# Performance work log

Measured on AMD Instinct MI355X. Metric: run time of the kernel, lower is better.

The kernel has to match this reference:

```python
import jax, jax.numpy as jnp
import numpy as np

NUM_HEADS = 16

def setup_inputs() -> dict:
    key = jax.random.key(0)
    ks = jax.random.split(key, 9)
    B, N, D = 4, 4096, 1024
    s = 1.0 / np.sqrt(D)
    return {
        "x": jax.random.normal(ks[0], (B, N, D), dtype=jnp.float32),
        "Wq": jax.random.normal(ks[1], (D, D), dtype=jnp.float32) * s,
        "bq": jnp.zeros((D,), dtype=jnp.float32),
        "Wk": jax.random.normal(ks[2], (D, D), dtype=jnp.float32) * s,
        "bk": jnp.zeros((D,), dtype=jnp.float32),
        "Wv": jax.random.normal(ks[3], (D, D), dtype=jnp.float32) * s,
        "bv": jnp.zeros((D,), dtype=jnp.float32),
        "Wp": jax.random.normal(ks[4], (D, D), dtype=jnp.float32) * s,
        "bp": jnp.zeros((D,), dtype=jnp.float32),
    }

def _split_heads(t, H):
    B, N, D = t.shape
    return t.reshape(B, N, H, D // H).transpose(0, 2, 1, 3)  # [B,H,N,hd]

def reference(x, Wq, bq, Wk, bk, Wv, bv, Wp, bp):
    H = NUM_HEADS
    q = jax.nn.elu(x @ Wq + bq) + 1.0   # elu feature map (config.elu=True)
    k = jax.nn.elu(x @ Wk + bk) + 1.0
    v = x @ Wv + bv
    q, k, v = _split_heads(q, H), _split_heads(k, H), _split_heads(v, H)
    # k^T v: [B,H,hd,hd]
    kv = jnp.einsum('bhnd,bhne->bhde', k, v)
    numerator = jnp.einsum('bhnd,bhde->bhne', q, kv)  # [B,H,N,hd]
    # adaptive normalizer: q @ sum_k
    sum_k = k.sum(axis=2)  # [B,H,hd]
    denominator = jnp.einsum('bhnd,bhd->bhn', q, sum_k)[..., None]
    y = numerator / denominator
    B, _, N, hd = y.shape
    y = y.transpose(0, 2, 1, 3).reshape(B, N, H * hd)
    return y @ Wp + bp
```

## Files before the change

kernel.cpp:

```cpp
#include <hip/hip_runtime.h>
#include <hip/hip_bf16.h>

typedef __attribute__((ext_vector_type(4))) float f32x4;
typedef __attribute__((ext_vector_type(4))) short s16x4;
typedef __attribute__((ext_vector_type(8))) short s16x8;
typedef __attribute__((ext_vector_type(8))) __bf16 bf16x8;

#define DEV static __device__ __forceinline__

DEV float bf2f(ushort u){
  unsigned x = ((unsigned)u) << 16;
  return __builtin_bit_cast(float, x);
}
DEV ushort f2bf(float f){
  unsigned x = __builtin_bit_cast(unsigned, f);
  x += 0x7fffu + ((x >> 16) & 1u);
  return (ushort)(x >> 16);
}
DEV void load_lds16(const void* g, void* l){
  __builtin_amdgcn_global_load_lds((const __attribute__((address_space(1))) void*)g,
                                   (__attribute__((address_space(3))) void*)l, 16, 0, 0);
}

__global__ __launch_bounds__(256) void k_prep(
    const float* __restrict__ x, ushort* __restrict__ xb,
    const float* __restrict__ Wq, const float* __restrict__ Wk,
    const float* __restrict__ Wv, const float* __restrict__ Wp,
    ushort* __restrict__ qkvT, ushort* __restrict__ wpT)
{
  __shared__ float tile[32][33];
  int bid = blockIdx.x, tid = threadIdx.x;
  if (bid < 8192) {
    int i = bid * 256 + tid;
    const f32x4* p = (const f32x4*)(x + (size_t)i * 8);
    f32x4 a = p[0], b = p[1];
    s16x8 o;
    o[0]=(short)f2bf(a[0]); o[1]=(short)f2bf(a[1]); o[2]=(short)f2bf(a[2]); o[3]=(short)f2bf(a[3]);
    o[4]=(short)f2bf(b[0]); o[5]=(short)f2bf(b[1]); o[6]=(short)f2bf(b[2]); o[7]=(short)f2bf(b[3]);
    *(s16x8*)(xb + (size_t)i * 8) = o;
  } else {
    int r = bid - 8192;
    int z = r >> 10; r &= 1023;
    const float* W = (z == 0) ? Wq : (z == 1) ? Wk : (z == 2) ? Wv : Wp;
    ushort* out = (z < 3) ? (qkvT + (size_t)z * 1024 * 1024) : wpT;
    int bx = (r & 31) * 32, by = (r >> 5) * 32;
    int tx = tid & 31, ty = tid >> 5;
    #pragma unroll
    for (int j = 0; j < 32; j += 8)
      tile[ty + j][tx] = W[(size_t)(by + ty + j) * 1024 + bx + tx];
    __syncthreads();
    #pragma unroll
    for (int j = 0; j < 32; j += 8)
      out[(size_t)(bx + ty + j) * 1024 + by + tx] = f2bf(tile[tx][ty + j]);
  }
}

template<int MODE>
__global__ __launch_bounds__(512, 1) void k_gemm(
    const ushort* __restrict__ A, const ushort* __restrict__ Bt,
    const float* __restrict__ b0, const float* __restrict__ b1, const float* __restrict__ b2,
    ushort* __restrict__ oQ, ushort* __restrict__ oK, ushort* __restrict__ oV,
    float* __restrict__ oF, int N)
{
  const int K = 1024;
  __shared__ ushort ldsA[2][16384];
  __shared__ ushort ldsB[2][16384];

  int wg = blockIdx.x;
  int cpx = gridDim.x >> 3;
  wg = (wg & 7) * cpx + (wg >> 3);
  int nbn = N >> 8;
  int bmi = wg / nbn, bni = wg - bmi * nbn;
  int m0 = bmi << 8, n0 = bni << 8;
  int tid = threadIdx.x, wid = tid >> 6, lane = tid & 63;
  int wr = wid >> 2, wc = wid & 3;
  int hi = lane >> 4, L = lane & 15;

  int rr = tid >> 3;
  int gaA = ((tid & 7) ^ (rr & 7)) << 3;
  int gaB = ((tid & 7) ^ ((tid >> 5) & 7)) << 3;
  const ushort* gA = A  + (size_t)(m0 + rr) * K + gaA;
  const ushort* gB = Bt + (size_t)(n0 + rr) * K + gaB;
  int ldst = wid << 10;

  int swz = (hi ^ (L & 7)) << 4;
  int arow = (wr * 128 + L) << 7;
  int brow = ((wc * 64 + L * 4)) << 7;

  f32x4 acc[8][4] = {};
  bf16x8 af[4], bf[4];

  #define RD_A(BASE, MH, KX)                                                   \
    _Pragma("unroll")                                                          \
    for (int m = 0; m < 4; ++m)                                                \
      af[m] = *(const bf16x8*)((BASE) + arow + (MH) * 8192 + (m << 11) + (swz ^ (KX)));
  #define RD_B(BASE, KX)                                                       \
    _Pragma("unroll")                                                          \
    for (int n = 0; n < 4; ++n)                                                \
      bf[n] = *(const bf16x8*)((BASE) + brow + (n << 7) + (swz ^ (KX)));
  #define MFMA16(MOFF)                                                         \
    _Pragma("unroll")                                                          \
    for (int m = 0; m < 4; ++m)                                                \
      _Pragma("unroll")                                                        \
      for (int n = 0; n < 4; ++n)                                              \
        acc[m + (MOFF)][n] =                                                   \
          __builtin_amdgcn_mfma_f32_16x16x32_bf16(af[m], bf[n], acc[m + (MOFF)][n], 0, 0, 0);

  #define ST_A0(SA_, kof) load_lds16(gA + (kof),                   (SA_) + ldst);
  #define ST_A1(SA_, kof) load_lds16(gA + (size_t) 64 * K + (kof), (SA_) + 8192  + ldst);
  #define ST_A2(SA_, kof) load_lds16(gA + (size_t)128 * K + (kof), (SA_) + 16384 + ldst);
  #define ST_A3(SA_, kof) load_lds16(gA + (size_t)192 * K + (kof), (SA_) + 24576 + ldst);
  #define ST_B0(SB_, kof) load_lds16(gB + (kof),                   (SB_) + ldst);
  #define ST_B1(SB_, kof) load_lds16(gB + (size_t) 64 * K + (kof), (SB_) + 8192  + ldst);
  #define ST_B2(SB_, kof) load_lds16(gB + (size_t)128 * K + (kof), (SB_) + 16384 + ldst);
  #define ST_B3(SB_, kof) load_lds16(gB + (size_t)192 * K + (kof), (SB_) + 24576 + ldst);

  #define PH8(LA_, LB_, MH, KX, MOFF, STG, WAIT)                               \
  { STG                                                                        \
    WAIT                                                                       \
    RD_A(LA_, MH, KX)                                                          \
    RD_B(LB_, KX)                                                              \
    asm volatile("s_waitcnt lgkmcnt(0)" ::: "memory");                         \
    __builtin_amdgcn_sched_barrier(0);                                         \
    __builtin_amdgcn_s_setprio(1);                                             \
    MFMA16(MOFF)                                                               \
    __builtin_amdgcn_s_setprio(0);                                             \
    __builtin_amdgcn_s_barrier(); }

  #define W2 { asm volatile("s_waitcnt vmcnt(2)" ::: "memory"); __builtin_amdgcn_s_barrier(); }
  #define W0 { asm volatile("s_waitcnt vmcnt(0)" ::: "memory"); __builtin_amdgcn_s_barrier(); }

  char* SA0 = (char*)&ldsA[0][0];
  char* SA1 = (char*)&ldsA[1][0];
  char* SB0 = (char*)&ldsB[0][0];
  char* SB1 = (char*)&ldsB[1][0];
  const char* LA0 = (const char*)&ldsA[0][0];
  const char* LA1 = (const char*)&ldsA[1][0];
  const char* LB0 = (const char*)&ldsB[0][0];
  const char* LB1 = (const char*)&ldsB[1][0];

  ST_A0(SA0, 0) ST_A1(SA0, 0) ST_A2(SA0, 0) ST_A3(SA0, 0)
  ST_B0(SB0, 0) ST_B1(SB0, 0) ST_B2(SB0, 0) ST_B3(SB0, 0)

  for (int i = 0; i < 7; ++i) {
    size_t ko  = (size_t)(2 * i + 1) << 6;
    size_t ke2 = (size_t)(2 * i + 2) << 6;
    PH8(LA0, LB0, 0, 0,  0, { ST_A1(SA1, ko) ST_A3(SA1, ko) }, W2)
    PH8(LA0, LB0, 0, 64, 0, { ST_A0(SA1, ko) ST_A2(SA1, ko) }, )
    PH8(LA0, LB0, 1, 64, 4, { ST_B0(SB1, ko) ST_B1(SB1, ko) }, )
    PH8(LA0, LB0, 1, 0,  4, { ST_B2(SB1, ko) ST_B3(SB1, ko) }, )
    PH8(LA1, LB1, 0, 0,  0, { ST_A1(SA0, ke2) ST_A3(SA0, ke2) }, W2)
    PH8(LA1, LB1, 0, 64, 0, { ST_A0(SA0, ke2) ST_A2(SA0, ke2) }, )
    PH8(LA1, LB1, 1, 64, 4, { ST_B0(SB0, ke2) ST_B1(SB0, ke2) }, )
    PH8(LA1, LB1, 1, 0,  4, { ST_B2(SB0, ke2) ST_B3(SB0, ke2) }, )
  }
  {
    size_t ko = (size_t)15 << 6;
    PH8(LA0, LB0, 0, 0,  0, { ST_A1(SA1, ko) ST_A3(SA1, ko) }, W2)
    PH8(LA0, LB0, 0, 64, 0, { ST_A0(SA1, ko) ST_A2(SA1, ko) }, )
    PH8(LA0, LB0, 1, 64, 4, { ST_B0(SB1, ko) ST_B1(SB1, ko) }, )
    PH8(LA0, LB0, 1, 0,  4, { ST_B2(SB1, ko) ST_B3(SB1, ko) }, )
    PH8(LA1, LB1, 0, 0,  0, { }, W0)
    PH8(LA1, LB1, 0, 64, 0, { }, )
    PH8(LA1, LB1, 1, 64, 4, { }, )
    PH8(LA1, LB1, 1, 0,  4, { }, )
  }
  #undef PH8
  #undef W2
  #undef W0
  #undef RD_A
  #undef RD_B
  #undef MFMA16

  int row0 = m0 + wr * 128 + (hi << 2);
  int cb4 = n0 + wc * 64 + (L << 2);
  if constexpr (MODE == 0) {
    f32x4 bias; ushort* dst; bool act;
    if (cb4 < 1024)      { bias = *(const f32x4*)(b0 + cb4);          dst = oQ + cb4;          act = true;  }
    else if (cb4 < 2048) { bias = *(const f32x4*)(b1 + (cb4 - 1024)); dst = oK + (cb4 - 1024); act = true;  }
    else                 { bias = *(const f32x4*)(b2 + (cb4 - 2048)); dst = oV + (cb4 - 2048); act = false; }
    #pragma unroll
    for (int m = 0; m < 8; ++m)
      #pragma unroll
      for (int j = 0; j < 4; ++j) {
        int r = row0 + m * 16 + j;
        s16x4 w;
        #pragma unroll
        for (int n = 0; n < 4; ++n) {
          float v = acc[m][n][j] + bias[n];
          if (act) v = (v > 0.f) ? (v + 1.f) : __expf(v);
          w[n] = (short)f2bf(v);
        }
        *(s16x4*)(dst + (size_t)r * 1024) = w;
      }
  } else {
    f32x4 bias = *(const f32x4*)(b0 + cb4);
    #pragma unroll
    for (int m = 0; m < 8; ++m)
      #pragma unroll
      for (int j = 0; j < 4; ++j) {
        int r = row0 + m * 16 + j;
        f32x4 w;
        #pragma unroll
        for (int n = 0; n < 4; ++n) w[n] = acc[m][n][j] + bias[n];
        *(f32x4*)(oF + (size_t)r * 1024 + cb4) = w;
      }
  }
}

__global__ __launch_bounds__(256, 2) void k_kv(
    const ushort* __restrict__ kbuf, const ushort* __restrict__ vbuf,
    float* __restrict__ kvp, float* __restrict__ skp)
{
  __shared__ ushort tile[2][8192];
  __shared__ float red[64 * 68];
  __shared__ float skred[4][64];

  int bh = blockIdx.x >> 3, chunk = blockIdx.x & 7;
  int b = bh >> 4, h = bh & 15;
  int tid = threadIdx.x, wid = tid >> 6, lane = tid & 63;
  int d0 = (lane >> 3) << 3, e0 = (lane & 7) << 3;

  size_t gbase = ((size_t)b * 4096 + chunk * 512 + wid * 16 + (lane >> 3)) * 1024
               + h * 64 + (lane & 7) * 8;

  float acc[8][8] = {};
  float sk[8] = {};

  #define STAGE_KV(bp, c)                                                     \
  { char* base_ = (char*)&tile[bp][0] + (wid << 11);                          \
    size_t g_ = gbase + (size_t)(c) * 65536;                                  \
    load_lds16(kbuf + g_,        base_);                                      \
    load_lds16(kbuf + g_ + 8192, base_ + 1024);                               \
    load_lds16(vbuf + g_,        base_ + 8192);                               \
    load_lds16(vbuf + g_ + 8192, base_ + 9216); }

  STAGE_KV(0, 0)

  for (int c = 0; c < 8; ++c) {
    if (c + 1 < 8) {
      STAGE_KV((c + 1) & 1, c + 1)
      asm volatile("s_waitcnt vmcnt(4)" ::: "memory");
    } else {
      asm volatile("s_waitcnt vmcnt(0)" ::: "memory");
    }
    __builtin_amdgcn_s_barrier();
    const ushort* Ks = &tile[c & 1][0];
    const ushort* Vs = &tile[c & 1][4096];
    #pragma unroll
    for (int t = 0; t < 16; ++t) {
      int nn = (wid << 4) + t;
      s16x8 k8 = *(const s16x8*)(Ks + nn * 64 + d0);
      s16x8 v8 = *(const s16x8*)(Vs + nn * 64 + e0);
      float kf[8], vf[8];
      #pragma unroll
      for (int i = 0; i < 8; ++i) { kf[i] = bf2f((ushort)k8[i]); vf[i] = bf2f((ushort)v8[i]); }
      #pragma unroll
      for (int i = 0; i < 8; ++i) {
        sk[i] += kf[i];
        #pragma unroll
        for (int j = 0; j < 8; ++j) acc[i][j] += kf[i] * vf[j];
      }
    }
    __builtin_amdgcn_sched_barrier(0);
    __builtin_amdgcn_s_barrier();
  }
  #undef STAGE_KV

  for (int w = 0; w < 4; ++w) {
    if (wid == w) {
      #pragma unroll
      for (int i = 0; i < 8; ++i)
        #pragma unroll
        for (int j4 = 0; j4 < 2; ++j4) {
          f32x4 v4;
          v4[0] = acc[i][j4 * 4 + 0]; v4[1] = acc[i][j4 * 4 + 1];
          v4[2] = acc[i][j4 * 4 + 2]; v4[3] = acc[i][j4 * 4 + 3];
          float* p = &red[(d0 + i) * 68 + e0 + j4 * 4];
          if (w == 0) *(f32x4*)p = v4;
          else        { f32x4 o = *(const f32x4*)p; *(f32x4*)p = o + v4; }
        }
    }
    __syncthreads();
  }

  size_t kvbase = ((size_t)chunk * 64 + bh) * 4096;
  #pragma unroll
  for (int i = 0; i < 16; ++i) {
    int el = tid + i * 256;
    kvp[kvbase + el] = red[(el >> 6) * 68 + (el & 63)];
  }
  if ((lane & 7) == 0) {
    #pragma unroll
    for (int i = 0; i < 8; ++i) skred[wid][d0 + i] = sk[i];
  }
  __syncthreads();
  if (tid < 64) {
    float s = 0.f;
    #pragma unroll
    for (int w = 0; w < 4; ++w) s += skred[w][tid];
    skp[(((size_t)chunk * 64 + bh) << 6) + tid] = s;
  }
}

__global__ __launch_bounds__(512, 2) void k_num(
    const ushort* __restrict__ qbuf, const float* __restrict__ kvp,
    const float* __restrict__ skp, ushort* __restrict__ ybuf)
{
  __shared__ float kvf[4096];
  __shared__ ushort kvtb[4096];
  __shared__ ushort skb[64];

  int bh = blockIdx.x >> 3, chunk = blockIdx.x & 7;
  int b = bh >> 4, h = bh & 15;
  int tid = threadIdx.x, wid = tid >> 6, lane = tid & 63;
  int hi = lane >> 4, L = lane & 15;

  #pragma unroll
  for (int i = 0; i < 2; ++i) {
    int i4 = tid + i * 512;
    f32x4 s = {0.f, 0.f, 0.f, 0.f};
    #pragma unroll
    for (int sl = 0; sl < 8; ++sl)
      s += *(const f32x4*)&kvp[(((size_t)sl * 64 + bh) << 12) + ((size_t)i4 << 2)];
    *(f32x4*)&kvf[i4 << 2] = s;
  }
  if (tid < 64) {
    float s = 0.f;
    #pragma unroll
    for (int sl = 0; sl < 8; ++sl) s += skp[(((size_t)sl * 64 + bh) << 6) + tid];
    skb[tid] = f2bf(s);
  }
  __syncthreads();
  {
    int e = tid >> 3, dg = tid & 7;
    s16x8 o;
    #pragma unroll
    for (int j = 0; j < 8; ++j) o[j] = (short)f2bf(kvf[(dg * 8 + j) * 64 + e]);
    *(s16x8*)((char*)kvtb + e * 128 + ((dg ^ (e & 7)) << 4)) = o;
  }
  __syncthreads();

  size_t r0 = (size_t)b * 4096 + chunk * 512 + wid * 64;
  const ushort* qb = qbuf + (r0 + L) * 1024 + h * 64 + hi * 8;

  f32x4 acc[4][4] = {};
  f32x4 accd[4] = {};
  #pragma unroll
  for (int kk = 0; kk < 2; ++kk) {
    bf16x8 bfr[4], bfd;
    bfd = *(const bf16x8*)((const char*)skb + kk * 64 + hi * 16);
    #pragma unroll
    for (int n = 0; n < 4; ++n) {
      int e = L * 4 + n;
      bfr[n] = *(const bf16x8*)((char*)kvtb + e * 128 + ((((kk << 2) | hi) ^ (e & 7)) << 4));
    }
    #pragma unroll
    for (int m = 0; m < 4; ++m) {
      bf16x8 af = *(const bf16x8*)(qb + (size_t)m * 16 * 1024 + kk * 32);
      #pragma unroll
      for (int n = 0; n < 4; ++n)
        acc[m][n] = __builtin_amdgcn_mfma_f32_16x16x32_bf16(af, bfr[n], acc[m][n], 0, 0, 0);
      accd[m] = __builtin_amdgcn_mfma_f32_16x16x32_bf16(af, bfd, accd[m], 0, 0, 0);
    }
  }

  #pragma unroll
  for (int m = 0; m < 4; ++m)
    #pragma unroll
    for (int j = 0; j < 4; ++j) {
      float inv = 1.0f / accd[m][j];
      s16x4 w;
      #pragma unroll
      for (int n = 0; n < 4; ++n) w[n] = (short)f2bf(acc[m][n][j] * inv);
      *(s16x4*)(ybuf + (r0 + m * 16 + hi * 4 + j) * 1024 + h * 64 + L * 4) = w;
    }
}

extern "C" void kernel_launch(void* const* d_in, const int* in_sizes, int n_in,
                              void* d_out, int out_size, void* d_ws, size_t ws_size,
                              hipStream_t stream)
{
  const float* x  = (const float*)d_in[0];
  const float* Wq = (const float*)d_in[1];
  const float* bq = (const float*)d_in[2];
  const float* Wk = (const float*)d_in[3];
  const float* bk = (const float*)d_in[4];
  const float* Wv = (const float*)d_in[5];
  const float* bv = (const float*)d_in[6];
  const float* Wp = (const float*)d_in[7];
  const float* bp = (const float*)d_in[8];

  char* ws = (char*)d_ws;
  ushort* xb    = (ushort*)(ws + 0);
  ushort* qkvT  = (ushort*)(ws + 33554432);
  ushort* wpT   = (ushort*)(ws + 39845888);
  ushort* ybuf  = (ushort*)(ws + 41943040);
  float*  kvp   = (float*)(ws + 0);
  float*  skp   = (float*)(ws + 8388608);

  ushort* vbuf = (ushort*)d_out;
  ushort* qbuf = (ushort*)d_out + 16777216;
  ushort* kbuf = ybuf;

  k_prep<<<12288, 256, 0, stream>>>(x, xb, Wq, Wk, Wv, Wp, qkvT, wpT);
  k_gemm<0><<<768, 512, 0, stream>>>(xb, qkvT, bq, bk, bv, qbuf, kbuf, vbuf, nullptr, 3072);
  k_kv<<<512, 256, 0, stream>>>(kbuf, vbuf, kvp, skp);
  k_num<<<512, 512, 0, stream>>>(qbuf, kvp, skp, ybuf);
  k_gemm<1><<<256, 512, 0, stream>>>(ybuf, wpT, bp, nullptr, nullptr,
                                     nullptr, nullptr, nullptr, (float*)d_out, 1024);
}
```

Before: 265.6 us.

## Restructure GEMM main loop into quadrant phases with deeper A prefetch

Reorganizes the 256x256 bf16 GEMM k-loop so each phase reads both k-halves of an A or B fragment set and issues MFMAs per output quadrant (8 phases per 2 k-tiles), reusing loaded fragments across phases. The global-to-LDS staging is rescheduled: A for the next tile is prefetched two tiles ahead, B loads are grouped, and vmcnt waits are moved to the end of phases. The aim is fewer LDS reads per MFMA and better overlap of global loads with compute, at the cost of more fragment registers and a more intricate barrier/wait ordering that could race if the counts are wrong.

```diff
diff --git a/kernel.cpp b/kernel.cpp
--- a/kernel.cpp
+++ b/kernel.cpp
@@ -88,47 +88,52 @@
   int brow = ((wc * 64 + L * 4)) << 7;
 
   f32x4 acc[8][4] = {};
-  bf16x8 af[4], bf[4];
-
-  #define RD_A(BASE, MH, KX)                                                   \
-    _Pragma("unroll")                                                          \
-    for (int m = 0; m < 4; ++m)                                                \
-      af[m] = *(const bf16x8*)((BASE) + arow + (MH) * 8192 + (m << 11) + (swz ^ (KX)));
-  #define RD_B(BASE, KX)                                                       \
-    _Pragma("unroll")                                                          \
-    for (int n = 0; n < 4; ++n)                                                \
-      bf[n] = *(const bf16x8*)((BASE) + brow + (n << 7) + (swz ^ (KX)));
-  #define MFMA16(MOFF)                                                         \
+  bf16x8 af[4][2];
+  bf16x8 bf[4][2];
+
+  #define RD_A(BASE, MH)                                                       \
     _Pragma("unroll")                                                          \
     for (int m = 0; m < 4; ++m)                                                \
       _Pragma("unroll")                                                        \
-      for (int n = 0; n < 4; ++n)                                              \
-        acc[m + (MOFF)][n] =                                                   \
-          __builtin_amdgcn_mfma_f32_16x16x32_bf16(af[m], bf[n], acc[m + (MOFF)][n], 0, 0, 0);
-
-  #define ST_A0(SA_, kof) load_lds16(gA + (kof),                   (SA_) + ldst);
-  #define ST_A1(SA_, kof) load_lds16(gA + (size_t) 64 * K + (kof), (SA_) + 8192  + ldst);
-  #define ST_A2(SA_, kof) load_lds16(gA + (size_t)128 * K + (kof), (SA_) + 16384 + ldst);
-  #define ST_A3(SA_, kof) load_lds16(gA + (size_t)192 * K + (kof), (SA_) + 24576 + ldst);
-  #define ST_B0(SB_, kof) load_lds16(gB + (kof),                   (SB_) + ldst);
-  #define ST_B1(SB_, kof) load_lds16(gB + (size_t) 64 * K + (kof), (SB_) + 8192  + ldst);
-  #define ST_B2(SB_, kof) load_lds16(gB + (size_t)128 * K + (kof), (SB_) + 16384 + ldst);
-  #define ST_B3(SB_, kof) load_lds16(gB + (size_t)192 * K + (kof), (SB_) + 24576 + ldst);
-
-  #define PH8(LA_, LB_, MH, KX, MOFF, STG, WAIT)                               \
-  { STG                                                                        \
-    WAIT                                                                       \
-    RD_A(LA_, MH, KX)                                                          \
-    RD_B(LB_, KX)                                                              \
+      for (int kk = 0; kk < 2; ++kk)                                           \
+        af[m][kk] = *(const bf16x8*)((BASE) + arow + (MH) * 8192 + (m << 11) + (swz ^ (kk << 6)));
+  #define RD_B(BASE, NH)                                                       \
+    _Pragma("unroll")                                                          \
+    for (int j = 0; j < 2; ++j)                                                \
+      _Pragma("unroll")                                                        \
+      for (int kk = 0; kk < 2; ++kk)                                           \
+        bf[(NH) * 2 + j][kk] = *(const bf16x8*)((BASE) + brow + (((NH) * 2 + j) << 7) + (swz ^ (kk << 6)));
+  #define MFMAQ(MH, NH)                                                        \
+    _Pragma("unroll")                                                          \
+    for (int m = 0; m < 4; ++m)                                                \
+      _Pragma("unroll")                                                        \
+      for (int j = 0; j < 2; ++j)                                              \
+        _Pragma("unroll")                                                      \
+        for (int kk = 0; kk < 2; ++kk)                                         \
+          acc[(MH) * 4 + m][(NH) * 2 + j] =                                    \
+            __builtin_amdgcn_mfma_f32_16x16x32_bf16(af[m][kk], bf[(NH) * 2 + j][kk], \
+                                                    acc[(MH) * 4 + m][(NH) * 2 + j], 0, 0, 0);
+
+  #define ST_A02(SA_, kof) { load_lds16(gA + (kof),                   (SA_) + ldst);          \
+                             load_lds16(gA + (size_t)128 * K + (kof), (SA_) + 16384 + ldst); }
+  #define ST_A13(SA_, kof) { load_lds16(gA + (size_t) 64 * K + (kof), (SA_) + 8192  + ldst);  \
+                             load_lds16(gA + (size_t)192 * K + (kof), (SA_) + 24576 + ldst); }
+  #define ST_B4(SB_, kof)  { load_lds16(gB + (kof),                   (SB_) + ldst);          \
+                             load_lds16(gB + (size_t) 64 * K + (kof), (SB_) + 8192  + ldst);  \
+                             load_lds16(gB + (size_t)128 * K + (kof), (SB_) + 16384 + ldst);  \
+                             load_lds16(gB + (size_t)192 * K + (kof), (SB_) + 24576 + ldst); }
+
+  #define PHASE(READS, STG, MFMAS, WAIT)                                       \
+  { READS                                                                      \
+    STG                                                                        \
+    __builtin_amdgcn_s_barrier();                                              \
     asm volatile("s_waitcnt lgkmcnt(0)" ::: "memory");                         \
     __builtin_amdgcn_sched_barrier(0);                                         \
     __builtin_amdgcn_s_setprio(1);                                             \
-    MFMA16(MOFF)                                                               \
+    MFMAS                                                                      \
     __builtin_amdgcn_s_setprio(0);                                             \
+    WAIT                                                                       \
     __builtin_amdgcn_s_barrier(); }
-
-  #define W2 { asm volatile("s_waitcnt vmcnt(2)" ::: "memory"); __builtin_amdgcn_s_barrier(); }
-  #define W0 { asm volatile("s_waitcnt vmcnt(0)" ::: "memory"); __builtin_amdgcn_s_barrier(); }
 
   char* SA0 = (char*)&ldsA[0][0];
   char* SA1 = (char*)&ldsA[1][0];
@@ -139,38 +144,33 @@
   const char* LB0 = (const char*)&ldsB[0][0];
   const char* LB1 = (const char*)&ldsB[1][0];
 
-  ST_A0(SA0, 0) ST_A1(SA0, 0) ST_A2(SA0, 0) ST_A3(SA0, 0)
-  ST_B0(SB0, 0) ST_B1(SB0, 0) ST_B2(SB0, 0) ST_B3(SB0, 0)
-
-  for (int i = 0; i < 7; ++i) {
+  ST_A02(SA0, 0) ST_A13(SA0, 0) ST_B4(SB0, 0)
+  ST_A02(SA1, 64) ST_A13(SA1, 64)
+  asm volatile("s_waitcnt vmcnt(4)" ::: "memory");
+  __builtin_amdgcn_s_barrier();
+
+  for (int i = 0; i < 8; ++i) {
     size_t ko  = (size_t)(2 * i + 1) << 6;
     size_t ke2 = (size_t)(2 * i + 2) << 6;
-    PH8(LA0, LB0, 0, 0,  0, { ST_A1(SA1, ko) ST_A3(SA1, ko) }, W2)
-    PH8(LA0, LB0, 0, 64, 0, { ST_A0(SA1, ko) ST_A2(SA1, ko) }, )
-    PH8(LA0, LB0, 1, 64, 4, { ST_B0(SB1, ko) ST_B1(SB1, ko) }, )
-    PH8(LA0, LB0, 1, 0,  4, { ST_B2(SB1, ko) ST_B3(SB1, ko) }, )
-    PH8(LA1, LB1, 0, 0,  0, { ST_A1(SA0, ke2) ST_A3(SA0, ke2) }, W2)
-    PH8(LA1, LB1, 0, 64, 0, { ST_A0(SA0, ke2) ST_A2(SA0, ke2) }, )
-    PH8(LA1, LB1, 1, 64, 4, { ST_B0(SB0, ke2) ST_B1(SB0, ke2) }, )
-    PH8(LA1, LB1, 1, 0,  4, { ST_B2(SB0, ke2) ST_B3(SB0, ke2) }, )
-  }
-  {
-    size_t ko = (size_t)15 << 6;
-    PH8(LA0, LB0, 0, 0,  0, { ST_A1(SA1, ko) ST_A3(SA1, ko) }, W2)
-    PH8(LA0, LB0, 0, 64, 0, { ST_A0(SA1, ko) ST_A2(SA1, ko) }, )
-    PH8(LA0, LB0, 1, 64, 4, { ST_B0(SB1, ko) ST_B1(SB1, ko) }, )
-    PH8(LA0, LB0, 1, 0,  4, { ST_B2(SB1, ko) ST_B3(SB1, ko) }, )
-    PH8(LA1, LB1, 0, 0,  0, { }, W0)
-    PH8(LA1, LB1, 0, 64, 0, { }, )
-    PH8(LA1, LB1, 1, 64, 4, { }, )
-    PH8(LA1, LB1, 1, 0,  4, { }, )
-  }
-  #undef PH8
-  #undef W2
-  #undef W0
+    size_t ko2 = (size_t)(2 * i + 3) << 6;
+    bool se = (2 * i + 2) < 16, so = (2 * i + 3) < 16;
+
+    PHASE( RD_A(LA0, 0) RD_B(LB0, 0), { ST_B4(SB1, ko) },          MFMAQ(0, 0), )
+    PHASE( RD_B(LB0, 1),              { if (se) ST_A02(SA0, ke2) }, MFMAQ(0, 1), )
+    PHASE( RD_A(LA0, 1),              { if (se) ST_B4(SB0, ke2) },  MFMAQ(1, 1), )
+    PHASE( ,                          { if (se) ST_A13(SA0, ke2) }, MFMAQ(1, 0),
+           { if (se) asm volatile("s_waitcnt vmcnt(8)" ::: "memory");
+             else    asm volatile("s_waitcnt vmcnt(0)" ::: "memory"); })
+    PHASE( RD_A(LA1, 0) RD_B(LB1, 0), ,                            MFMAQ(0, 0), )
+    PHASE( RD_B(LB1, 1),              { if (so) ST_A02(SA1, ko2) }, MFMAQ(0, 1), )
+    PHASE( RD_A(LA1, 1),              ,                            MFMAQ(1, 1), )
+    PHASE( ,                          { if (so) ST_A13(SA1, ko2) }, MFMAQ(1, 0),
+           { if (so) asm volatile("s_waitcnt vmcnt(4)" ::: "memory"); })
+  }
+  #undef PHASE
   #undef RD_A
   #undef RD_B
-  #undef MFMA16
+  #undef MFMAQ
 
   int row0 = m0 + wr * 128 + (hi << 2);
   int cb4 = n0 + wc * 64 + (L << 2);
```

Measured after the change: 242.6 us. 8.7% less time.
